# Kernel optimization log

Hardware: AMD Instinct MI355X
Metric: run time of the kernel (lower is better)

The kernel has to match this reference:

```python
import jax, jax.numpy as jnp
import numpy as np

NUM_BINS = 8
TAIL = 3.0
MIN_BW = 1e-3   # min_bin_width
MIN_BH = 1e-3   # min_bin_height
MIN_D = 1e-3    # min_derivative
EPS = 1e-6      # searchsorted eps
N = 4_194_304


def setup_inputs() -> dict:
    key = jax.random.key(0)
    k1, k2 = jax.random.split(key)
    inputs = jax.random.normal(k1, (N,), dtype=jnp.float32)
    params = jax.random.normal(k2, (N, 3 * NUM_BINS + 1), dtype=jnp.float32)
    return {"inputs": inputs, "params": params}


def _cum_knots(unnorm, min_size):
    # softmax * 2B, then affine rescale (faithful to the torch source, even
    # though it is a nonstandard normalization), cumsum, pad with -B, pin last to B.
    B, K = TAIL, NUM_BINS
    w = jax.nn.softmax(unnorm, axis=-1) * (2.0 * B)
    w = w * (2.0 * B - K * min_size) + min_size
    c = jnp.cumsum(w, axis=-1)
    c = jnp.concatenate([jnp.full(c.shape[:-1] + (1,), -B, c.dtype), c], axis=-1)
    return c.at[..., -1].set(B)


def _gather(a, idx):
    return jnp.take_along_axis(a, idx[:, None], axis=-1)[:, 0]


def reference(inputs, params):
    K, B = NUM_BINS, TAIL
    x = inputs.reshape(-1)
    uw = params[..., :K]
    uh = params[..., K:2 * K]
    ud = params[..., 2 * K:]              # [N, K+1]

    inside = (x >= -B) & (x <= B)
    # clamp for the spline branch so masked-out lanes stay finite (identical
    # math for inside elements)
    xi = jnp.clip(x, -B, B)

    cumwidths = _cum_knots(uw, MIN_BW)     # [N, K+1]
    cumheights = _cum_knots(uh, MIN_BH)    # [N, K+1]
    derivs = jax.nn.softplus(ud) + MIN_D   # [N, K+1]

    # searchsorted: last knot nudged by eps, count of (x >= knot) - 1
    bin_loc = cumwidths.at[..., -1].add(EPS)
    idx = jnp.sum((xi[:, None] >= bin_loc).astype(jnp.int32), axis=-1) - 1
    idx = jnp.clip(idx, 0, K - 1)

    cw_k = _gather(cumwidths, idx)
    cw_k1 = _gather(cumwidths, idx + 1)
    ch_k = _gather(cumheights, idx)
    ch_k1 = _gather(cumheights, idx + 1)
    d_k = _gather(derivs, idx)
    d_k1 = _gather(derivs, idx + 1)

    bw = cw_k1 - cw_k
    bh = ch_k1 - ch_k
    theta = (xi - cw_k) / bw
    t1m = theta * (1.0 - theta)
    numerator = bh * (d_k * theta ** 2 + d_k1 * t1m)
    denominator = d_k * theta ** 2 + 2.0 * d_k1 * t1m + (1.0 - theta) ** 2
    out_inside = ch_k + numerator / denominator
    deriv_numerator = d_k1 * d_k * bh * denominator ** 2
    ld_inside = jnp.log(deriv_numerator / (bw * denominator ** 2))

    # outside the interval: identity with log|det| = log(first derivative)
    ld_outside = jnp.log(derivs[..., 0])

    outputs = jnp.where(inside, out_inside, x)
    log_abs_det = jnp.where(inside, ld_inside, ld_outside)
    return outputs.reshape(inputs.shape), log_abs_det.sum()
```

## Files before the change

kernel.cpp:

```cpp
#include <hip/hip_runtime.h>
#include <math.h>


#define TAILB 3.0f
#define MINSZ 0.001f

typedef unsigned int u32;

__device__ __forceinline__ void gload_lds16(const void* g, void* l) {
    __builtin_amdgcn_global_load_lds(
        (const __attribute__((address_space(1))) u32*)g,
        (__attribute__((address_space(3))) u32*)l,
        16, 0, 0);
}

__device__ __forceinline__ float frcp(float x) {
    return __builtin_amdgcn_rcpf(x);
}

__device__ __forceinline__ float softplus_d(float u) {
    return fmaxf(u, 0.0f) + __logf(1.0f + __expf(-fabsf(u))) + MINSZ;
}

__launch_bounds__(256, 6)
__global__ void rqs_kernel(const float* __restrict__ x_in,
                           const float* __restrict__ params,
                           float* __restrict__ out,
                           float* __restrict__ partial)
{
    __shared__ __align__(16) float lds[256 * 25];
    __shared__ float wsum[4];

    const int tid = threadIdx.x;
    const int bid = blockIdx.x;
    const int i = bid * 256 + tid;

    const float x = x_in[i];

    const float4* src = (const float4*)params + (size_t)bid * 1600;
    float4* dst = (float4*)lds;
    #pragma unroll
    for (int v = 0; v < 6; ++v) {
        const int q = tid + v * 256;
        gload_lds16(src + q, dst + q);
    }
    if (tid < 64) {
        const int q = tid + 1536;
        gload_lds16(src + q, dst + q);
    }

    const float xi = fminf(fmaxf(x, -TAILB), TAILB);
    __syncthreads();

    const float* row = &lds[tid * 25];
    const float fac_num = (2.0f * TAILB) * (2.0f * TAILB - 8.0f * MINSZ);

    float ew[8];
    float s = 0.0f;
    #pragma unroll
    for (int j = 0; j < 8; ++j) { ew[j] = __expf(row[j]); s += ew[j]; }
    const float facw = fac_num * frcp(s);

    float c = 0.0f;
    int idx = 0;
    float cw_k = -TAILB, cw_k1 = TAILB;
    bool found = false;
    #pragma unroll
    for (int j = 0; j < 7; ++j) {
        c = fmaf(ew[j], facw, c + MINSZ);
        const bool ge = (xi >= c);
        idx += ge ? 1 : 0;
        cw_k  = ge ? c : cw_k;
        cw_k1 = (!ge && !found) ? c : cw_k1;
        found = found || !ge;
    }

    float ch_k = -TAILB, ch_k1 = TAILB;
    {
        float eh[8];
        float sh = 0.0f;
        #pragma unroll
        for (int j = 0; j < 8; ++j) { eh[j] = __expf(row[8 + j]); sh += eh[j]; }
        const float fach = fac_num * frcp(sh);
        c = 0.0f;
        #pragma unroll
        for (int j = 1; j <= 7; ++j) {
            c = fmaf(eh[j - 1], fach, c + MINSZ);
            ch_k  = (idx == j)     ? c : ch_k;
            ch_k1 = (idx + 1 == j) ? c : ch_k1;
        }
    }

    const float d_k  = softplus_d(row[16 + idx]);
    const float d_k1 = softplus_d(row[17 + idx]);

    const float bw  = cw_k1 - cw_k;
    const float bh  = ch_k1 - ch_k;
    const float rbw = frcp(bw);
    const float th  = (xi - cw_k) * rbw;
    const float omt = 1.0f - th;
    const float th2 = th * th;
    const float t1m = th * omt;
    const float num = bh * fmaf(d_k, th2, d_k1 * t1m);
    const float den = fmaf(2.0f * d_k1, t1m, fmaf(d_k, th2, omt * omt));
    const float out_in = fmaf(num, frcp(den), ch_k);

    const bool inside = (x >= -TAILB) && (x <= TAILB);
    out[i] = inside ? out_in : x;

    float ldarg = d_k1 * d_k * bh * rbw;
    if (!__all(inside)) {
        const float d0 = softplus_d(row[16]);
        ldarg = inside ? ldarg : d0;
    }
    const float ldv = __logf(ldarg);

    float acc = ldv;
    #pragma unroll
    for (int off = 32; off > 0; off >>= 1)
        acc += __shfl_down(acc, off);
    const int wave = tid >> 6, lane = tid & 63;
    if (lane == 0) wsum[wave] = acc;
    __syncthreads();
    if (tid == 0)
        partial[bid] = (wsum[0] + wsum[1]) + (wsum[2] + wsum[3]);
}

__global__ void rqs_reduce(const float* __restrict__ partial, int nb,
                           float* __restrict__ out_sum)
{
    const int tid = threadIdx.x;
    const int nb4 = nb >> 2;
    const float4* p4 = (const float4*)partial;
    double acc = 0.0;
    for (int q = tid; q < nb4; q += 1024) {
        float4 v = p4[q];
        acc += (double)v.x + (double)v.y + (double)v.z + (double)v.w;
    }
    #pragma unroll
    for (int off = 32; off > 0; off >>= 1)
        acc += __shfl_down(acc, off);
    __shared__ double wsum[16];
    const int wave = tid >> 6, lane = tid & 63;
    if (lane == 0) wsum[wave] = acc;
    __syncthreads();
    if (tid == 0) {
        double t = 0.0;
        #pragma unroll
        for (int w = 0; w < 16; ++w) t += wsum[w];
        *out_sum = (float)t;
    }
}

extern "C" void kernel_launch(void* const* d_in, const int* in_sizes, int n_in,
                              void* d_out, int out_size, void* d_ws, size_t ws_size,
                              hipStream_t stream) {
    const float* x      = (const float*)d_in[0];
    const float* params = (const float*)d_in[1];
    float* out = (float*)d_out;
    const int n = in_sizes[0];
    const int nb = n / 256;
    float* partial = (float*)d_ws;

    hipLaunchKernelGGL(rqs_kernel, dim3(nb), dim3(256), 0, stream,
                       x, params, out, partial);
    hipLaunchKernelGGL(rqs_reduce, dim3(1), dim3(1024), 0, stream,
                       partial, nb, out + n);
}
```

Before: 87.29 us.

## Convert to persistent double-buffered kernel staging params and x into LDS

Replaces the one-block-per-tile launch with 768 persistent blocks that loop over tiles, prefetching the next tile's params and x into a second LDS buffer via direct global-to-LDS loads while computing the current one. Each block accumulates its log-det in registers and writes one partial, so the final reduce handles 768 values. The intent is to hide memory latency and cut per-block launch and reduction overhead. In exchange, LDS per block doubles (occupancy drops to 3 blocks), and the schedule relies on a hand-written vmcnt wait and raw barriers being correct. It also hardcodes the tile count, so it only works for this N.

```diff
diff --git a/kernel.cpp b/kernel.cpp
--- a/kernel.cpp
+++ b/kernel.cpp
@@ -4,6 +4,11 @@
 
 #define TAILB 3.0f
 #define MINSZ 0.001f
+#define NBLOCKS 768
+#define NTILES 16384
+#define TILE_F4 1600
+#define BUF_F4 1664
+#define BUF_F 6656
 
 typedef unsigned int u32;
 
@@ -22,100 +27,122 @@
     return fmaxf(u, 0.0f) + __logf(1.0f + __expf(-fabsf(u))) + MINSZ;
 }
 
-__launch_bounds__(256, 6)
+__device__ __forceinline__ void stage_tile(const float4* __restrict__ params4,
+                                           const float4* __restrict__ x4,
+                                           float4* ldsbuf, int tile, int tid)
+{
+    const float4* psrc = params4 + (size_t)tile * TILE_F4;
+    #pragma unroll
+    for (int v = 0; v < 6; ++v) {
+        const int q = tid + v * 256;
+        gload_lds16(psrc + q, ldsbuf + q);
+    }
+    const int q = 1536 + tid;
+    if (q < 1600) {
+        gload_lds16(psrc + q, ldsbuf + q);
+    } else if (q < 1664) {
+        gload_lds16(x4 + (size_t)tile * 64 + (q - 1600), ldsbuf + q);
+    } else {
+        gload_lds16(psrc + tid, ldsbuf + tid);
+    }
+}
+
+__launch_bounds__(256, 3)
 __global__ void rqs_kernel(const float* __restrict__ x_in,
                            const float* __restrict__ params,
                            float* __restrict__ out,
                            float* __restrict__ partial)
 {
-    __shared__ __align__(16) float lds[256 * 25];
+    __shared__ __align__(16) float lds[2 * BUF_F];
     __shared__ float wsum[4];
 
     const int tid = threadIdx.x;
     const int bid = blockIdx.x;
-    const int i = bid * 256 + tid;
+    const float4* params4 = (const float4*)params;
+    const float4* x4 = (const float4*)x_in;
+    const float fac_num = (2.0f * TAILB) * (2.0f * TAILB - 8.0f * MINSZ);
 
-    const float x = x_in[i];
+    float accv = 0.0f;
 
-    const float4* src = (const float4*)params + (size_t)bid * 1600;
-    float4* dst = (float4*)lds;
-    #pragma unroll
-    for (int v = 0; v < 6; ++v) {
-        const int q = tid + v * 256;
-        gload_lds16(src + q, dst + q);
-    }
-    if (tid < 64) {
-        const int q = tid + 1536;
-        gload_lds16(src + q, dst + q);
+    stage_tile(params4, x4, (float4*)lds, bid, tid);
+
+    int k = 0;
+    for (int t = bid; t < NTILES; t += NBLOCKS, ++k) {
+        const int cur = k & 1;
+        const int tn = (t + NBLOCKS < NTILES) ? (t + NBLOCKS) : t;
+        stage_tile(params4, x4, (float4*)&lds[(cur ^ 1) * BUF_F], tn, tid);
+
+        asm volatile("s_waitcnt vmcnt(7)" ::: "memory");
+        __builtin_amdgcn_s_barrier();
+
+        const float* row = &lds[cur * BUF_F + tid * 25];
+        const float x = lds[cur * BUF_F + 6400 + tid];
+        const float xi = fminf(fmaxf(x, -TAILB), TAILB);
+
+        float ew[8];
+        float s = 0.0f;
+        #pragma unroll
+        for (int j = 0; j < 8; ++j) { ew[j] = __expf(row[j]); s += ew[j]; }
+        const float facw = fac_num * frcp(s);
+
+        float c = 0.0f;
+        int idx = 0;
+        float cw_k = -TAILB, cw_k1 = TAILB;
+        bool found = false;
+        #pragma unroll
+        for (int j = 0; j < 7; ++j) {
+            c = fmaf(ew[j], facw, c + MINSZ);
+            const bool ge = (xi >= c);
+            idx += ge ? 1 : 0;
+            cw_k  = ge ? c : cw_k;
+            cw_k1 = (!ge && !found) ? c : cw_k1;
+            found = found || !ge;
+        }
+
+        float ch_k = -TAILB, ch_k1 = TAILB;
+        {
+            float eh[8];
+            float sh = 0.0f;
+            #pragma unroll
+            for (int j = 0; j < 8; ++j) { eh[j] = __expf(row[8 + j]); sh += eh[j]; }
+            const float fach = fac_num * frcp(sh);
+            c = 0.0f;
+            #pragma unroll
+            for (int j = 1; j <= 7; ++j) {
+                c = fmaf(eh[j - 1], fach, c + MINSZ);
+                ch_k  = (idx == j)     ? c : ch_k;
+                ch_k1 = (idx + 1 == j) ? c : ch_k1;
+            }
+        }
+
+        const float d_k  = softplus_d(row[16 + idx]);
+        const float d_k1 = softplus_d(row[17 + idx]);
+
+        const float bw  = cw_k1 - cw_k;
+        const float bh  = ch_k1 - ch_k;
+        const float rbw = frcp(bw);
+        const float th  = (xi - cw_k) * rbw;
+        const float omt = 1.0f - th;
+        const float th2 = th * th;
+        const float t1m = th * omt;
+        const float num = bh * fmaf(d_k, th2, d_k1 * t1m);
+        const float den = fmaf(2.0f * d_k1, t1m, fmaf(d_k, th2, omt * omt));
+        const float out_in = fmaf(num, frcp(den), ch_k);
+
+        const bool inside = (x >= -TAILB) && (x <= TAILB);
+        __builtin_nontemporal_store(inside ? out_in : x, &out[t * 256 + tid]);
+
+        float ldarg = d_k1 * d_k * bh * rbw;
+        if (!__all(inside)) {
+            const float d0 = softplus_d(row[16]);
+            ldarg = inside ? ldarg : d0;
+        }
+        accv += __logf(ldarg);
+
+        __builtin_amdgcn_s_barrier();
     }
 
-    const float xi = fminf(fmaxf(x, -TAILB), TAILB);
-    __syncthreads();
-
-    const float* row = &lds[tid * 25];
-    const float fac_num = (2.0f * TAILB) * (2.0f * TAILB - 8.0f * MINSZ);
-
-    float ew[8];
-    float s = 0.0f;
-    #pragma unroll
-    for (int j = 0; j < 8; ++j) { ew[j] = __expf(row[j]); s += ew[j]; }
-    const float facw = fac_num * frcp(s);
-
-    float c = 0.0f;
-    int idx = 0;
-    float cw_k = -TAILB, cw_k1 = TAILB;
-    bool found = false;
-    #pragma unroll
-    for (int j = 0; j < 7; ++j) {
-        c = fmaf(ew[j], facw, c + MINSZ);
-        const bool ge = (xi >= c);
-        idx += ge ? 1 : 0;
-        cw_k  = ge ? c : cw_k;
-        cw_k1 = (!ge && !found) ? c : cw_k1;
-        found = found || !ge;
-    }
-
-    float ch_k = -TAILB, ch_k1 = TAILB;
-    {
-        float eh[8];
-        float sh = 0.0f;
-        #pragma unroll
-        for (int j = 0; j < 8; ++j) { eh[j] = __expf(row[8 + j]); sh += eh[j]; }
-        const float fach = fac_num * frcp(sh);
-        c = 0.0f;
-        #pragma unroll
-        for (int j = 1; j <= 7; ++j) {
-            c = fmaf(eh[j - 1], fach, c + MINSZ);
-            ch_k  = (idx == j)     ? c : ch_k;
-            ch_k1 = (idx + 1 == j) ? c : ch_k1;
-        }
-    }
-
-    const float d_k  = softplus_d(row[16 + idx]);
-    const float d_k1 = softplus_d(row[17 + idx]);
-
-    const float bw  = cw_k1 - cw_k;
-    const float bh  = ch_k1 - ch_k;
-    const float rbw = frcp(bw);
-    const float th  = (xi - cw_k) * rbw;
-    const float omt = 1.0f - th;
-    const float th2 = th * th;
-    const float t1m = th * omt;
-    const float num = bh * fmaf(d_k, th2, d_k1 * t1m);
-    const float den = fmaf(2.0f * d_k1, t1m, fmaf(d_k, th2, omt * omt));
-    const float out_in = fmaf(num, frcp(den), ch_k);
-
-    const bool inside = (x >= -TAILB) && (x <= TAILB);
-    out[i] = inside ? out_in : x;
-
-    float ldarg = d_k1 * d_k * bh * rbw;
-    if (!__all(inside)) {
-        const float d0 = softplus_d(row[16]);
-        ldarg = inside ? ldarg : d0;
-    }
-    const float ldv = __logf(ldarg);
-
-    float acc = ldv;
+    float acc = accv;
     #pragma unroll
     for (int off = 32; off > 0; off >>= 1)
         acc += __shfl_down(acc, off);
@@ -130,26 +157,18 @@
                            float* __restrict__ out_sum)
 {
     const int tid = threadIdx.x;
-    const int nb4 = nb >> 2;
-    const float4* p4 = (const float4*)partial;
     double acc = 0.0;
-    for (int q = tid; q < nb4; q += 1024) {
-        float4 v = p4[q];
-        acc += (double)v.x + (double)v.y + (double)v.z + (double)v.w;
-    }
+    for (int q = tid; q < nb; q += 256)
+        acc += (double)partial[q];
     #pragma unroll
     for (int off = 32; off > 0; off >>= 1)
         acc += __shfl_down(acc, off);
-    __shared__ double wsum[16];
+    __shared__ double wsum[4];
     const int wave = tid >> 6, lane = tid & 63;
     if (lane == 0) wsum[wave] = acc;
     __syncthreads();
-    if (tid == 0) {
-        double t = 0.0;
-        #pragma unroll
-        for (int w = 0; w < 16; ++w) t += wsum[w];
-        *out_sum = (float)t;
-    }
+    if (tid == 0)
+        *out_sum = (float)((wsum[0] + wsum[1]) + (wsum[2] + wsum[3]));
 }
 
 extern "C" void kernel_launch(void* const* d_in, const int* in_sizes, int n_in,
@@ -159,11 +178,10 @@
     const float* params = (const float*)d_in[1];
     float* out = (float*)d_out;
     const int n = in_sizes[0];
-    const int nb = n / 256;
     float* partial = (float*)d_ws;
 
-    hipLaunchKernelGGL(rqs_kernel, dim3(nb), dim3(256), 0, stream,
+    hipLaunchKernelGGL(rqs_kernel, dim3(NBLOCKS), dim3(256), 0, stream,
                        x, params, out, partial);
-    hipLaunchKernelGGL(rqs_reduce, dim3(1), dim3(1024), 0, stream,
-                       partial, nb, out + n);
+    hipLaunchKernelGGL(rqs_reduce, dim3(1), dim3(256), 0, stream,
+                       partial, NBLOCKS, out + n);
 }
```

After: 89.15 us. +2.1%, slower.

## Load parameter rows directly from global memory instead of staging through LDS

Applied to the files above, without the earlier changes.

Removes the async global-to-LDS staging of each block's 25-float parameter rows and the barrier after it. Each thread now reads its own width and height logits with four 16-byte loads, plus only the two derivative logits it needs, selected by bin index. The output store is made nontemporal. This saves LDS space and a sync, which may raise occupancy, but the per-thread loads are strided and not 16-byte aligned, so coalescing may get worse. The whole rows are still pulled through the cache either way.

```diff
diff --git a/kernel.cpp b/kernel.cpp
--- a/kernel.cpp
+++ b/kernel.cpp
@@ -4,15 +4,6 @@
 
 #define TAILB 3.0f
 #define MINSZ 0.001f
-
-typedef unsigned int u32;
-
-__device__ __forceinline__ void gload_lds16(const void* g, void* l) {
-    __builtin_amdgcn_global_load_lds(
-        (const __attribute__((address_space(1))) u32*)g,
-        (__attribute__((address_space(3))) u32*)l,
-        16, 0, 0);
-}
 
 __device__ __forceinline__ float frcp(float x) {
     return __builtin_amdgcn_rcpf(x);
@@ -28,37 +19,30 @@
                            float* __restrict__ out,
                            float* __restrict__ partial)
 {
-    __shared__ __align__(16) float lds[256 * 25];
     __shared__ float wsum[4];
 
     const int tid = threadIdx.x;
     const int bid = blockIdx.x;
     const int i = bid * 256 + tid;
 
+    const float* rp = params + (size_t)i * 25;
+
     const float x = x_in[i];
-
-    const float4* src = (const float4*)params + (size_t)bid * 1600;
-    float4* dst = (float4*)lds;
-    #pragma unroll
-    for (int v = 0; v < 6; ++v) {
-        const int q = tid + v * 256;
-        gload_lds16(src + q, dst + q);
-    }
-    if (tid < 64) {
-        const int q = tid + 1536;
-        gload_lds16(src + q, dst + q);
-    }
+    float w0[4], w1[4], h0[4], h1[4];
+    __builtin_memcpy(&w0, rp +  0, 16);
+    __builtin_memcpy(&w1, rp +  4, 16);
+    __builtin_memcpy(&h0, rp +  8, 16);
+    __builtin_memcpy(&h1, rp + 12, 16);
 
     const float xi = fminf(fmaxf(x, -TAILB), TAILB);
-    __syncthreads();
-
-    const float* row = &lds[tid * 25];
     const float fac_num = (2.0f * TAILB) * (2.0f * TAILB - 8.0f * MINSZ);
 
     float ew[8];
     float s = 0.0f;
     #pragma unroll
-    for (int j = 0; j < 8; ++j) { ew[j] = __expf(row[j]); s += ew[j]; }
+    for (int j = 0; j < 4; ++j) { ew[j]     = __expf(w0[j]); s += ew[j]; }
+    #pragma unroll
+    for (int j = 0; j < 4; ++j) { ew[4 + j] = __expf(w1[j]); s += ew[4 + j]; }
     const float facw = fac_num * frcp(s);
 
     float c = 0.0f;
@@ -75,12 +59,17 @@
         found = found || !ge;
     }
 
+    const float ud_k  = rp[16 + idx];
+    const float ud_k1 = rp[17 + idx];
+
     float ch_k = -TAILB, ch_k1 = TAILB;
     {
         float eh[8];
         float sh = 0.0f;
         #pragma unroll
-        for (int j = 0; j < 8; ++j) { eh[j] = __expf(row[8 + j]); sh += eh[j]; }
+        for (int j = 0; j < 4; ++j) { eh[j]     = __expf(h0[j]); sh += eh[j]; }
+        #pragma unroll
+        for (int j = 0; j < 4; ++j) { eh[4 + j] = __expf(h1[j]); sh += eh[4 + j]; }
         const float fach = fac_num * frcp(sh);
         c = 0.0f;
         #pragma unroll
@@ -91,8 +80,8 @@
         }
     }
 
-    const float d_k  = softplus_d(row[16 + idx]);
-    const float d_k1 = softplus_d(row[17 + idx]);
+    const float d_k  = softplus_d(ud_k);
+    const float d_k1 = softplus_d(ud_k1);
 
     const float bw  = cw_k1 - cw_k;
     const float bh  = ch_k1 - ch_k;
@@ -106,11 +95,11 @@
     const float out_in = fmaf(num, frcp(den), ch_k);
 
     const bool inside = (x >= -TAILB) && (x <= TAILB);
-    out[i] = inside ? out_in : x;
+    __builtin_nontemporal_store(inside ? out_in : x, &out[i]);
 
     float ldarg = d_k1 * d_k * bh * rbw;
     if (!__all(inside)) {
-        const float d0 = softplus_d(row[16]);
+        const float d0 = softplus_d(rp[16]);
         ldarg = inside ? ldarg : d0;
     }
     const float ldv = __logf(ldarg);
```

New measurement: 96.59 us. 1.11x slower.
